# Optimization experiments

Measured on AMD Instinct MI355X. Metric: run time of the kernel, lower is better.

Reference implementation:

```python
import jax, jax.numpy as jnp
import numpy as np

TOPK = 6
ROUTE_SCALE = 1.5


def setup_inputs() -> dict:
    key = jax.random.key(0)
    k1, k2, k3 = jax.random.split(key, 3)
    N, D, E = 16384, 4096, 256
    x = jax.random.normal(k1, (N, D), dtype=jnp.float32)
    weight = jax.random.normal(k2, (E, D), dtype=jnp.float32) * (D ** -0.5)
    bias = jax.random.normal(k3, (E,), dtype=jnp.float32) * 0.02
    return {"x": x, "weight": weight, "bias": bias}


def reference(x, weight, bias):
    # gate linear: [N, D] @ [E, D]^T -> [N, E], computed in fp32
    scores = jnp.einsum('nd,ed->ne', x.astype(jnp.float32), weight.astype(jnp.float32))
    # sqrtsoftplus score function
    original_scores = jnp.sqrt(jax.nn.softplus(scores))
    # bias only affects expert selection, not the routing weights
    biased = original_scores + bias
    _, indices = jax.lax.top_k(biased, TOPK)          # [N, TOPK] int32
    weights = jnp.take_along_axis(original_scores, indices, axis=-1)
    # non-softmax score func -> renormalize selected weights
    weights = weights / jnp.sum(weights, axis=-1, keepdims=True)
    weights = weights * ROUTE_SCALE
    return weights, indices
```

## Files before the change

kernel.cpp:

```cpp
#include <hip/hip_runtime.h>
#include <math.h>

constexpr int D     = 4096;
constexpr int D4    = 1024;
constexpr int E     = 256;
constexpr int TK    = 6;
constexpr int BM    = 64;
constexpr int NT    = 1024;
constexpr int CK    = 512;
constexpr int NCH   = D / CK;
constexpr int NST   = CK / 32;
constexpr float TAU = 3e-5f;

typedef __attribute__((ext_vector_type(8)))  short short8;
typedef __attribute__((ext_vector_type(16))) float float16;
typedef unsigned short ushort_t;

__device__ __forceinline__ ushort_t f2bf(float f) {
  unsigned u = __float_as_uint(f);
  return (ushort_t)((u + 0x7fffu + ((u >> 16) & 1u)) >> 16);
}
__device__ __forceinline__ float bf2f(ushort_t h) {
  return __uint_as_float(((unsigned)h) << 16);
}

struct __align__(16) SMem {
  union {
    struct {
      ushort_t A2[BM * 1024];
    } st;
    struct {
      float red[8][2][16][64];
      float val[BM * 65];
      int   id [BM * 65];
    } ep;
  } u;
  float  bias[E];
  int    nflag;
  int    flagrow[BM];
  int    flagid[BM][8];
  double exact[8];
};
static_assert(sizeof(SMem) <= 160 * 1024, "LDS overflow");

__global__ __launch_bounds__(256)
void conv_w(const float* __restrict__ wg, ushort_t* __restrict__ whi,
            ushort_t* __restrict__ wlo)
{
  size_t i = (size_t)blockIdx.x * 256 + threadIdx.x;
  const int e  = (int)(i >> 10);
  const int k4 = (int)(i & 1023);
  const int kt = k4 >> 3;
  const int kw = (k4 & 7) * 4;
  float4 v = ((const float4*)wg)[i];
  float a[4] = {v.x, v.y, v.z, v.w};
  ushort_t h[4], l[4];
#pragma unroll
  for (int j = 0; j < 4; ++j) {
    h[j] = f2bf(a[j]);
    l[j] = f2bf(a[j] - bf2f(h[j]));
  }
  const size_t dst = (size_t)kt * (E * 32) + e * 32 + kw;
  *(uint2*)&whi[dst] = *(uint2*)h;
  *(uint2*)&wlo[dst] = *(uint2*)l;
}

__global__ __launch_bounds__(NT, 4)
void gate_kernel(const float* __restrict__ xg, const float* __restrict__ wg,
                 const float* __restrict__ bg,
                 const ushort_t* __restrict__ whi, const ushort_t* __restrict__ wlo,
                 float* __restrict__ outw, float* __restrict__ outi)
{
  __shared__ SMem sm;
  const int t    = threadIdx.x;
  const int row0 = blockIdx.x * BM;
  const int wv   = t >> 6;
  const int lane = t & 63;
  const int m    = lane & 31;
  const int hf   = lane >> 5;
  const int eg   = wv >> 1;
  const int kh   = wv & 1;

  if (t < E) sm.bias[t] = bg[t];
  if (t == 0) sm.nflag = 0;

  const float4* x4 = (const float4*)xg;
  const float4* w4 = (const float4*)wg;

  float16 acc0, acc1;
#pragma unroll
  for (int i = 0; i < 16; ++i) { acc0[i] = 0.f; acc1[i] = 0.f; }

  const int a_row = t >> 4;
  const int kc    = t & 15;

  const int q  = kh * 2 + hf;
  const int b2 = (m >> 2) & 1;
  const ushort_t* a0P = &sm.u.st.A2[m        * 1024 + ((q ^ (m & 3)) << 3)];
  const ushort_t* a1P = &sm.u.st.A2[(32 + m) * 1024 + ((q ^ (m & 3)) << 3)];

  const size_t bOff = (size_t)(eg * 32 + m) * 32 + kh * 16 + hf * 8;

  auto stage_A = [&](int c) {
    const float4* src = x4 + (size_t)(row0 + a_row) * D4 + c * 128 + kc;
#pragma unroll
    for (int j = 0; j < 8; ++j) {
      float4 v = src[j * 16];
      float a[4] = {v.x, v.y, v.z, v.w};
      ushort_t h[4], l[4];
#pragma unroll
      for (int i = 0; i < 4; ++i) {
        h[i] = f2bf(a[i]);
        l[i] = f2bf(a[i] - bf2f(h[i]));
      }
      const int slot = j * 8 + (kc >> 1);
      const int half = kc & 1;
      const int sw   = ((slot ^ (a_row & 7)) << 3) + half * 4;
      *(uint2*)&sm.u.st.A2[a_row * 1024 + sw]       = *(uint2*)h;
      *(uint2*)&sm.u.st.A2[a_row * 1024 + 512 + sw] = *(uint2*)l;
    }
  };

  for (int c = 0; c < NCH; ++c) {
    __syncthreads();
    stage_A(c);
    __syncthreads();

    const ushort_t* bH = whi + (size_t)(c * NST) * 8192 + bOff;
    const ushort_t* bL = wlo + (size_t)(c * NST) * 8192 + bOff;
#pragma unroll 4
    for (int s = 0; s < NST; ++s) {
      short8 bh = *(const short8*)(bH + (size_t)s * 8192);
      short8 bl = *(const short8*)(bL + (size_t)s * 8192);
      const int ao = (s ^ b2) << 5;
      short8 a0h = *(const short8*)(a0P + ao);
      short8 a0l = *(const short8*)(a0P + 512 + ao);
      short8 a1h = *(const short8*)(a1P + ao);
      short8 a1l = *(const short8*)(a1P + 512 + ao);
      acc0 = __builtin_amdgcn_mfma_f32_32x32x16_bf16(a0h, bh, acc0, 0, 0, 0);
      acc0 = __builtin_amdgcn_mfma_f32_32x32x16_bf16(a0h, bl, acc0, 0, 0, 0);
      acc0 = __builtin_amdgcn_mfma_f32_32x32x16_bf16(a0l, bh, acc0, 0, 0, 0);
      acc1 = __builtin_amdgcn_mfma_f32_32x32x16_bf16(a1h, bh, acc1, 0, 0, 0);
      acc1 = __builtin_amdgcn_mfma_f32_32x32x16_bf16(a1h, bl, acc1, 0, 0, 0);
      acc1 = __builtin_amdgcn_mfma_f32_32x32x16_bf16(a1l, bh, acc1, 0, 0, 0);
    }
  }

  __syncthreads();

  if (kh == 1) {
#pragma unroll
    for (int r = 0; r < 16; ++r) {
      sm.u.ep.red[eg][0][r][lane] = acc0[r];
      sm.u.ep.red[eg][1][r][lane] = acc1[r];
    }
  }
  __syncthreads();
  if (kh == 0) {
#pragma unroll
    for (int r = 0; r < 16; ++r) {
      acc0[r] += sm.u.ep.red[eg][0][r][lane];
      acc1[r] += sm.u.ep.red[eg][1][r][lane];
    }
  }

  const int myE = eg * 32 + m;
  const float myBias = sm.bias[myE];

  if (kh == 0) {
#pragma unroll
    for (int b = 0; b < 2; ++b) {
#pragma unroll
      for (int reg = 0; reg < 16; ++reg) {
        const int row_local = b * 32 + (reg & 3) + 8 * (reg >> 2) + 4 * hf;
        float s = b ? acc1[reg] : acc0[reg];
        float v = sqrtf(fmaxf(s, 0.f) + log1pf(expf(-fabsf(s)))) + myBias;
#pragma unroll
        for (int ssel = 0; ssel < 8; ++ssel) {
          float bv = v;
#pragma unroll
          for (int off = 1; off < 32; off <<= 1)
            bv = fmaxf(bv, __shfl_xor(bv, off, 64));
          unsigned long long ball = __ballot(v == bv);
          unsigned hm = (unsigned)(ball >> (hf * 32));
          int mwin = __ffs(hm) - 1;
          if (m == mwin) {
            sm.u.ep.val[row_local * 65 + eg * 8 + ssel] = v;
            sm.u.ep.id [row_local * 65 + eg * 8 + ssel] = myE;
            v = -INFINITY;
          }
        }
      }
    }
  }
  __syncthreads();

  if (t < 512) {
    const int r = t >> 3, g = t & 7;
    float mv[8]; int mi[8];
#pragma unroll
    for (int q2 = 0; q2 < 8; ++q2) {
      mv[q2] = sm.u.ep.val[r * 65 + q2 * 8 + g];
      mi[q2] = sm.u.ep.id [r * 65 + q2 * 8 + g];
    }
    float tv[8]; int ti[8];
#pragma unroll
    for (int s = 0; s < 8; ++s) {
      float bv = mv[0]; int bi = mi[0];
#pragma unroll
      for (int q2 = 1; q2 < 8; ++q2)
        if (mv[q2] > bv || (mv[q2] == bv && mi[q2] < bi)) { bv = mv[q2]; bi = mi[q2]; }
#pragma unroll
      for (int off = 1; off < 8; off <<= 1) {
        float ov = __shfl_xor(bv, off, 64);
        int   oi = __shfl_xor(bi, off, 64);
        if (ov > bv || (ov == bv && oi < bi)) { bv = ov; bi = oi; }
      }
      tv[s] = bv; ti[s] = bi;
#pragma unroll
      for (int q2 = 0; q2 < 8; ++q2)
        if (mi[q2] == bi) mv[q2] = -INFINITY;
    }
    if (g == 0) {
      bool flag = false;
#pragma unroll
      for (int i = 0; i < 7; ++i) flag |= (tv[i] - tv[i + 1] < TAU);
      const int grow = row0 + r;
      if (!flag) {
        float og[6], ssum = 0.f;
#pragma unroll
        for (int i = 0; i < 6; ++i) { og[i] = tv[i] - sm.bias[ti[i]]; ssum += og[i]; }
        const float sc = 1.5f / ssum;
#pragma unroll
        for (int i = 0; i < 6; ++i) {
          outw[(size_t)grow * TK + i] = og[i] * sc;
          outi[(size_t)grow * TK + i] = (float)ti[i];
        }
      } else {
        int slot = atomicAdd(&sm.nflag, 1);
        sm.flagrow[slot] = grow;
#pragma unroll
        for (int i = 0; i < 8; ++i) sm.flagid[slot][i] = ti[i];
      }
    }
  }
  __syncthreads();

  const int nf = sm.nflag;
  for (int f = 0; f < nf; ++f) {
    const int grow = sm.flagrow[f];
    if (wv < 8) {
      const int e = sm.flagid[f][wv];
      double accd = 0.0;
      const float4* xr = x4 + (size_t)grow * D4 + lane * 16;
      const float4* wr = w4 + (size_t)e    * D4 + lane * 16;
#pragma unroll
      for (int i = 0; i < 16; ++i) {
        float4 xv = xr[i], wl = wr[i];
        accd = fma((double)xv.x, (double)wl.x, accd);
        accd = fma((double)xv.y, (double)wl.y, accd);
        accd = fma((double)xv.z, (double)wl.z, accd);
        accd = fma((double)xv.w, (double)wl.w, accd);
      }
#pragma unroll
      for (int off = 1; off < 64; off <<= 1)
        accd += __shfl_xor(accd, off, 64);
      if (lane == 0) {
        double sp = fmax(accd, 0.0) + log1p(exp(-fabs(accd)));
        sm.exact[wv] = sqrt(sp);
      }
    }
    __syncthreads();
    if (t == 0) {
      double ov[8]; int oid[8], ordr[8];
      for (int i = 0; i < 8; ++i) { ov[i] = sm.exact[i]; oid[i] = sm.flagid[f][i]; ordr[i] = i; }
      for (int i = 0; i < 6; ++i) {
        int b = i;
        for (int j = i + 1; j < 8; ++j) {
          double bj = ov[ordr[j]] + (double)sm.bias[oid[ordr[j]]];
          double bb = ov[ordr[b]] + (double)sm.bias[oid[ordr[b]]];
          if (bj > bb || (bj == bb && oid[ordr[j]] < oid[ordr[b]])) b = j;
        }
        int tmp = ordr[i]; ordr[i] = ordr[b]; ordr[b] = tmp;
      }
      double ssum = 0.0;
      for (int i = 0; i < 6; ++i) ssum += ov[ordr[i]];
      double sc = 1.5 / ssum;
      for (int i = 0; i < 6; ++i) {
        outw[(size_t)grow * TK + i] = (float)(ov[ordr[i]] * sc);
        outi[(size_t)grow * TK + i] = (float)oid[ordr[i]];
      }
    }
    __syncthreads();
  }
}

extern "C" void kernel_launch(void* const* d_in, const int* in_sizes, int n_in,
                              void* d_out, int out_size, void* d_ws, size_t ws_size,
                              hipStream_t stream) {
  const float* x = (const float*)d_in[0];
  const float* w = (const float*)d_in[1];
  const float* b = (const float*)d_in[2];
  float* out  = (float*)d_out;
  const int N = in_sizes[0] / D;

  ushort_t* whi = (ushort_t*)d_ws;
  ushort_t* wlo = whi + (size_t)E * D;

  float* outw = out;
  float* outi = out + (size_t)N * TK;

  hipLaunchKernelGGL(conv_w, dim3(E * D / 4 / 256), dim3(256), 0, stream,
                     w, whi, wlo);
  hipLaunchKernelGGL(gate_kernel, dim3(N / BM), dim3(NT), 0, stream,
                     x, w, b, whi, wlo, outw, outi);
}
```

Before: 552.7 us.

## Replace shuffle-based per-group top-8 selection with bitonic key sort network

The epilogue now writes all 256 biased scores per row to LDS and has 16 threads per row each sort 16 packed (value,index) 64-bit keys with a sorting network. Bitonic merges across shuffles then produce the row's top-8. This replaces the earlier 8-round wavefront max/ballot selection per group, which needed many shuffles per element. The split-K reduction add is also folded into the score computation. In exchange it uses 64-bit shuffles and more registers per thread, and the LDS value buffer gets larger.

```diff
diff --git a/kernel.cpp b/kernel.cpp
--- a/kernel.cpp
+++ b/kernel.cpp
@@ -10,11 +10,13 @@
 constexpr int CK    = 512;
 constexpr int NCH   = D / CK;
 constexpr int NST   = CK / 32;
+constexpr int VST   = 260;
 constexpr float TAU = 3e-5f;
 
 typedef __attribute__((ext_vector_type(8)))  short short8;
 typedef __attribute__((ext_vector_type(16))) float float16;
 typedef unsigned short ushort_t;
+typedef unsigned long long u64;
 
 __device__ __forceinline__ ushort_t f2bf(float f) {
   unsigned u = __float_as_uint(f);
@@ -23,6 +25,34 @@
 __device__ __forceinline__ float bf2f(ushort_t h) {
   return __uint_as_float(((unsigned)h) << 16);
 }
+
+__device__ __forceinline__ u64 mkkey(float v, int idx) {
+  unsigned u = __float_as_uint(v);
+  u = ((int)u < 0) ? ~u : (u | 0x80000000u);
+  return ((u64)u << 32) | (unsigned)(255 - idx);
+}
+__device__ __forceinline__ float keyval(u64 k) {
+  unsigned u = (unsigned)(k >> 32);
+  return __uint_as_float((u & 0x80000000u) ? (u & 0x7FFFFFFFu) : ~u);
+}
+__device__ __forceinline__ int keyidx(u64 k) {
+  return 255 - (int)(unsigned)(k & 0xFFFFFFFFu);
+}
+__device__ __forceinline__ u64 kmax(u64 a, u64 b) { return a < b ? b : a; }
+
+#define CEK(i, j) do { u64 _a = k[i], _b = k[j]; bool _p = _a < _b;          \
+                       k[i] = _p ? _b : _a; k[j] = _p ? _a : _b; } while (0)
+#define SORT8(b) do {                                                        \
+  CEK(b+0,b+1); CEK(b+2,b+3); CEK(b+4,b+5); CEK(b+6,b+7);                    \
+  CEK(b+0,b+2); CEK(b+1,b+3); CEK(b+4,b+6); CEK(b+5,b+7);                    \
+  CEK(b+1,b+2); CEK(b+5,b+6);                                                \
+  CEK(b+0,b+4); CEK(b+1,b+5); CEK(b+2,b+6); CEK(b+3,b+7);                    \
+  CEK(b+2,b+4); CEK(b+3,b+5);                                                \
+  CEK(b+1,b+2); CEK(b+3,b+4); CEK(b+5,b+6); } while (0)
+#define BMERGE8 do {                                                         \
+  CEK(0,4); CEK(1,5); CEK(2,6); CEK(3,7);                                    \
+  CEK(0,2); CEK(1,3); CEK(4,6); CEK(5,7);                                    \
+  CEK(0,1); CEK(2,3); CEK(4,5); CEK(6,7); } while (0)
 
 struct __align__(16) SMem {
   union {
@@ -31,8 +61,7 @@
     } st;
     struct {
       float red[8][2][16][64];
-      float val[BM * 65];
-      int   id [BM * 65];
+      float val[BM * VST];
     } ep;
   } u;
   float  bias[E];
@@ -156,72 +185,60 @@
     }
   }
   __syncthreads();
+
   if (kh == 0) {
-#pragma unroll
-    for (int r = 0; r < 16; ++r) {
-      acc0[r] += sm.u.ep.red[eg][0][r][lane];
-      acc1[r] += sm.u.ep.red[eg][1][r][lane];
-    }
-  }
-
-  const int myE = eg * 32 + m;
-  const float myBias = sm.bias[myE];
-
-  if (kh == 0) {
+    const int myE = eg * 32 + m;
+    const float myBias = sm.bias[myE];
 #pragma unroll
     for (int b = 0; b < 2; ++b) {
 #pragma unroll
       for (int reg = 0; reg < 16; ++reg) {
         const int row_local = b * 32 + (reg & 3) + 8 * (reg >> 2) + 4 * hf;
-        float s = b ? acc1[reg] : acc0[reg];
+        float s = (b ? acc1[reg] : acc0[reg]) +
+                  sm.u.ep.red[eg][b][reg][lane];
         float v = sqrtf(fmaxf(s, 0.f) + log1pf(expf(-fabsf(s)))) + myBias;
-#pragma unroll
-        for (int ssel = 0; ssel < 8; ++ssel) {
-          float bv = v;
-#pragma unroll
-          for (int off = 1; off < 32; off <<= 1)
-            bv = fmaxf(bv, __shfl_xor(bv, off, 64));
-          unsigned long long ball = __ballot(v == bv);
-          unsigned hm = (unsigned)(ball >> (hf * 32));
-          int mwin = __ffs(hm) - 1;
-          if (m == mwin) {
-            sm.u.ep.val[row_local * 65 + eg * 8 + ssel] = v;
-            sm.u.ep.id [row_local * 65 + eg * 8 + ssel] = myE;
-            v = -INFINITY;
-          }
-        }
+        sm.u.ep.val[row_local * VST + myE] = v;
       }
     }
   }
   __syncthreads();
 
-  if (t < 512) {
-    const int r = t >> 3, g = t & 7;
-    float mv[8]; int mi[8];
-#pragma unroll
-    for (int q2 = 0; q2 < 8; ++q2) {
-      mv[q2] = sm.u.ep.val[r * 65 + q2 * 8 + g];
-      mi[q2] = sm.u.ep.id [r * 65 + q2 * 8 + g];
-    }
-    float tv[8]; int ti[8];
-#pragma unroll
-    for (int s = 0; s < 8; ++s) {
-      float bv = mv[0]; int bi = mi[0];
-#pragma unroll
-      for (int q2 = 1; q2 < 8; ++q2)
-        if (mv[q2] > bv || (mv[q2] == bv && mi[q2] < bi)) { bv = mv[q2]; bi = mi[q2]; }
-#pragma unroll
-      for (int off = 1; off < 8; off <<= 1) {
-        float ov = __shfl_xor(bv, off, 64);
-        int   oi = __shfl_xor(bi, off, 64);
-        if (ov > bv || (ov == bv && oi < bi)) { bv = ov; bi = oi; }
-      }
-      tv[s] = bv; ti[s] = bi;
-#pragma unroll
-      for (int q2 = 0; q2 < 8; ++q2)
-        if (mi[q2] == bi) mv[q2] = -INFINITY;
-    }
-    if (g == 0) {
+  {
+    const int r  = t >> 4;
+    const int sl = t & 15;
+    const float* vr = &sm.u.ep.val[r * VST + sl * 16];
+    u64 k[16];
+#pragma unroll
+    for (int j = 0; j < 4; ++j) {
+      float4 q4 = *(const float4*)&vr[j * 4];
+      k[j * 4 + 0] = mkkey(q4.x, sl * 16 + j * 4 + 0);
+      k[j * 4 + 1] = mkkey(q4.y, sl * 16 + j * 4 + 1);
+      k[j * 4 + 2] = mkkey(q4.z, sl * 16 + j * 4 + 2);
+      k[j * 4 + 3] = mkkey(q4.w, sl * 16 + j * 4 + 3);
+    }
+    SORT8(0);
+    SORT8(8);
+    k[0] = kmax(k[0], k[15]); k[1] = kmax(k[1], k[14]);
+    k[2] = kmax(k[2], k[13]); k[3] = kmax(k[3], k[12]);
+    k[4] = kmax(k[4], k[11]); k[5] = kmax(k[5], k[10]);
+    k[6] = kmax(k[6], k[9]);  k[7] = kmax(k[7], k[8]);
+    BMERGE8;
+#pragma unroll
+    for (int off = 1; off < 16; off <<= 1) {
+      u64 o[8];
+#pragma unroll
+      for (int i = 0; i < 8; ++i) o[i] = __shfl_xor(k[i], off, 64);
+      k[0] = kmax(k[0], o[7]); k[1] = kmax(k[1], o[6]);
+      k[2] = kmax(k[2], o[5]); k[3] = kmax(k[3], o[4]);
+      k[4] = kmax(k[4], o[3]); k[5] = kmax(k[5], o[2]);
+      k[6] = kmax(k[6], o[1]); k[7] = kmax(k[7], o[0]);
+      BMERGE8;
+    }
+
+    if (sl == 0) {
+      float tv[8]; int ti[8];
+#pragma unroll
+      for (int i = 0; i < 8; ++i) { tv[i] = keyval(k[i]); ti[i] = keyidx(k[i]); }
       bool flag = false;
 #pragma unroll
       for (int i = 0; i < 7; ++i) flag |= (tv[i] - tv[i + 1] < TAU);
```

Result: faster. 497.9 us (-9.9%).
